# Performance work log

Measured on AMD Instinct MI355X. Metric: run time of the kernel, lower is better.

## Reference

```python
import jax, jax.numpy as jnp
import numpy as np

NUM_EXPERTS = 8
TOP_K = 2
D_IN = 1024
D_OUT = 1024
N_TOKENS = 8192


def setup_inputs() -> dict:
    key = jax.random.key(0)
    ks = jax.random.split(key, 7)
    s_in = 1.0 / np.sqrt(D_IN)
    s_out = 1.0 / np.sqrt(D_OUT)
    return {
        "x": jax.random.normal(ks[0], (N_TOKENS, D_IN), dtype=jnp.float32),
        # stacked expert params: fc1 [E, D_in, D_out], fc2 [E, D_out, D_out]
        "W1": jax.random.uniform(ks[1], (NUM_EXPERTS, D_IN, D_OUT), jnp.float32, -s_in, s_in),
        "b1": jax.random.uniform(ks[2], (NUM_EXPERTS, D_OUT), jnp.float32, -s_in, s_in),
        "W2": jax.random.uniform(ks[3], (NUM_EXPERTS, D_OUT, D_OUT), jnp.float32, -s_out, s_out),
        "b2": jax.random.uniform(ks[4], (NUM_EXPERTS, D_OUT), jnp.float32, -s_out, s_out),
        "Wg": jax.random.uniform(ks[5], (D_IN, NUM_EXPERTS), jnp.float32, -s_in, s_in),
        "bg": jax.random.uniform(ks[6], (NUM_EXPERTS,), jnp.float32, -s_in, s_in),
    }


def reference(x, W1, b1, W2, b2, Wg, bg):
    n = x.shape[0]
    # gating
    gate_logits = x @ Wg + bg                      # [N, E]
    gate_weights = jax.nn.softmax(gate_logits, axis=1)
    if TOP_K < NUM_EXPERTS:
        topk_vals, topk_idx = jax.lax.top_k(gate_weights, TOP_K)  # [N, K]
        rows = jnp.arange(n)[:, None]
        gate_weights = jnp.zeros_like(gate_weights).at[rows, topk_idx].set(topk_vals)
    # dense all-expert MLP fan-out (faithful to the original wasteful compute)
    h = jax.nn.relu(jnp.einsum('nd,edh->enh', x, W1) + b1[:, None, :])  # [E, N, H]
    y = jnp.einsum('enh,eho->eno', h, W2) + b2[:, None, :]               # [E, N, O]
    # weighted combine over experts
    out = jnp.einsum('ne,eno->no', gate_weights, y)                      # [N, O]
    return out
```

## Files before the change

kernel.cpp:

```cpp
#include <hip/hip_runtime.h>

#define NUM_E 8
#define N_TOK 8192
#define DIM 1024

typedef __attribute__((ext_vector_type(8))) short short8;
typedef __attribute__((ext_vector_type(4))) float f32x4;

__device__ __forceinline__ unsigned short f2bf(float f) {
  unsigned int u = __float_as_uint(f);
  u = (u + 0x7fffu + ((u >> 16) & 1u)) >> 16;
  return (unsigned short)u;
}

__device__ __forceinline__ void async16(const unsigned short* g, unsigned short* l) {
  __builtin_amdgcn_global_load_lds((const __attribute__((address_space(1))) void*)g,
                                   (__attribute__((address_space(3))) void*)l,
                                   16, 0, 0);
}

__global__ __launch_bounds__(256) void prep_kernel(
    const float* __restrict__ W1, const float* __restrict__ W2,
    unsigned short* __restrict__ W1T, unsigned short* __restrict__ W2T,
    const float* __restrict__ x, const float* __restrict__ Wg,
    const float* __restrict__ bg, int* __restrict__ tok_top,
    float2* __restrict__ tok_wts, unsigned short* __restrict__ xb) {
  __shared__ float s[64][65];
  if (blockIdx.x < 4096) {
    const int bx  = blockIdx.x;
    const int mat = bx >> 8;
    const int tk  = (bx >> 4) & 15;
    const int tn  = bx & 15;
    const float* src;
    unsigned short* dst;
    if (mat < 8) { src = W1 + (size_t)mat * (DIM * DIM); dst = W1T + (size_t)mat * (DIM * DIM); }
    else         { src = W2 + (size_t)(mat - 8) * (DIM * DIM); dst = W2T + (size_t)(mat - 8) * (DIM * DIM); }
    const int k0 = tk * 64, n0 = tn * 64;
    const int t = threadIdx.x;
    const int nr = t & 63, wr = t >> 6;
#pragma unroll
    for (int i = 0; i < 16; ++i) {
      int k = i * 4 + wr;
      s[nr][k] = src[(size_t)(k0 + k) * DIM + n0 + nr];
    }
    __syncthreads();
    const int kq = (t & 15) * 4, nw = t >> 4;
#pragma unroll
    for (int i = 0; i < 4; ++i) {
      int n = i * 16 + nw;
      ushort4 o;
      o.x = f2bf(s[n][kq + 0]); o.y = f2bf(s[n][kq + 1]);
      o.z = f2bf(s[n][kq + 2]); o.w = f2bf(s[n][kq + 3]);
      *(ushort4*)(dst + (size_t)(n0 + n) * DIM + k0 + kq) = o;
    }
  } else {
    const int wave = threadIdx.x >> 6;
    const int lane = threadIdx.x & 63;
    const int n = (blockIdx.x - 4096) * 4 + wave;
    const float4* xr = (const float4*)(x + (size_t)n * DIM);
    unsigned short* xbr = xb + (size_t)n * DIM;
    float acc[NUM_E];
#pragma unroll
    for (int e = 0; e < NUM_E; ++e) acc[e] = 0.f;
#pragma unroll
    for (int it = 0; it < 4; ++it) {
      float4 xv = xr[it * 64 + lane];
      const float4* wr = (const float4*)Wg + (size_t)(it * 256 + lane * 4) * 2;
      float xs[4] = {xv.x, xv.y, xv.z, xv.w};
      union { unsigned short u[4]; uint2 v; } oo;
      oo.u[0] = f2bf(xv.x); oo.u[1] = f2bf(xv.y);
      oo.u[2] = f2bf(xv.z); oo.u[3] = f2bf(xv.w);
      *(uint2*)(xbr + it * 256 + lane * 4) = oo.v;
#pragma unroll
      for (int dd = 0; dd < 4; ++dd) {
        float4 wa = wr[dd * 2 + 0];
        float4 wb = wr[dd * 2 + 1];
        acc[0] += xs[dd] * wa.x; acc[1] += xs[dd] * wa.y;
        acc[2] += xs[dd] * wa.z; acc[3] += xs[dd] * wa.w;
        acc[4] += xs[dd] * wb.x; acc[5] += xs[dd] * wb.y;
        acc[6] += xs[dd] * wb.z; acc[7] += xs[dd] * wb.w;
      }
    }
#pragma unroll
    for (int e = 0; e < NUM_E; ++e)
#pragma unroll
      for (int off = 32; off > 0; off >>= 1)
        acc[e] += __shfl_down(acc[e], off);
    if (lane == 0) {
      float p[NUM_E];
      float mx = -1e30f;
#pragma unroll
      for (int e = 0; e < NUM_E; ++e) { p[e] = acc[e] + bg[e]; mx = fmaxf(mx, p[e]); }
      float ss = 0.f;
#pragma unroll
      for (int e = 0; e < NUM_E; ++e) { p[e] = expf(p[e] - mx); ss += p[e]; }
      float inv = 1.f / ss;
      int i0 = 0;
#pragma unroll
      for (int e = 1; e < NUM_E; ++e) if (p[e] > p[i0]) i0 = e;
      int i1 = (i0 == 0) ? 1 : 0;
#pragma unroll
      for (int e = 0; e < NUM_E; ++e) if (e != i0 && p[e] > p[i1]) i1 = e;
      tok_top[n] = i0 | (i1 << 8);
      tok_wts[n] = make_float2(p[i0] * inv, p[i1] * inv);
    }
  }
}

__global__ __launch_bounds__(1024) void gate2_kernel(const int* __restrict__ tok_top,
                                                     const float2* __restrict__ tok_wts,
                                                     int* __restrict__ counts,
                                                     int* __restrict__ tok_idx,
                                                     float* __restrict__ tok_w) {
  const int e = blockIdx.x;
  const int t = threadIdx.x;
  const int lane = t & 63;
  const int wave = t >> 6;
  __shared__ int wsum[16];
  __shared__ int blocktot;
  int match[8];
  float w[8];
  int cnt = 0;
#pragma unroll
  for (int j = 0; j < 8; ++j) {
    int n = t * 8 + j;
    int top = tok_top[n];
    float2 ww = tok_wts[n];
    bool m0 = (top & 0xff) == e;
    bool m1 = ((top >> 8) & 0xff) == e;
    match[j] = (m0 || m1) ? 1 : 0;
    w[j] = m0 ? ww.x : ww.y;
    cnt += match[j];
  }
  int inc = cnt;
#pragma unroll
  for (int off = 1; off < 64; off <<= 1) {
    int v = __shfl_up(inc, off);
    if (lane >= off) inc += v;
  }
  if (lane == 63) wsum[wave] = inc;
  __syncthreads();
  if (t < 16) {
    int v = wsum[t];
    int s = v;
#pragma unroll
    for (int off = 1; off < 16; off <<= 1) {
      int u = __shfl_up(s, off);
      if (lane >= off) s += u;
    }
    wsum[t] = s - v;
    if (t == 15) blocktot = s;
  }
  __syncthreads();
  int slot = wsum[wave] + inc - cnt;
#pragma unroll
  for (int j = 0; j < 8; ++j) {
    if (match[j]) {
      tok_idx[e * N_TOK + slot] = t * 8 + j;
      tok_w[e * N_TOK + slot] = w[j];
      slot++;
    }
  }
  if (t == 0) counts[e] = blocktot;
}


template <bool FC1>
__global__ __launch_bounds__(256, 3) void moe_gemm_kernel(
    const unsigned short* __restrict__ A_src,
    const unsigned short* __restrict__ wT,
    const float* __restrict__ bias,
    const int* __restrict__ counts,
    const int* __restrict__ tok_idx,
    const float* __restrict__ tok_w,
    unsigned short* __restrict__ h_out,
    float* __restrict__ out)
{
  const int y = blockIdx.y;
  int e = -1, m0 = 0, base = 0;
  {
    int acc_tiles = 0, acc_rows = 0;
#pragma unroll
    for (int i = 0; i < NUM_E; ++i) {
      int c = counts[i];
      int t = (c + 127) >> 7;
      if (y >= acc_tiles && y < acc_tiles + t) {
        e = i; m0 = (y - acc_tiles) * 128; base = acc_rows;
      }
      acc_tiles += t;
      acc_rows += t * 128;
    }
  }
  if (e < 0) return;
  const int count = counts[e];
  const int n0 = blockIdx.x * 128;

  const int tid  = threadIdx.x;
  const int wave = tid >> 6;
  const int lane = tid & 63;
  const int l15  = lane & 15;
  const int quad = lane >> 4;
  const int wm   = wave & 1;
  const int wn   = wave >> 1;

  __shared__ unsigned short sA[2 * 4096];
  __shared__ unsigned short sB[2 * 4096];
  __shared__ int   s_tok[128];
  __shared__ float s_w[128];

  if (!FC1 && tid < 128) {
    int slot = m0 + tid;
    int cs = slot < count ? slot : count - 1;
    s_tok[tid] = tok_idx[e * N_TOK + cs];
    s_w[tid]   = slot < count ? tok_w[e * N_TOK + slot] : 0.f;
  }

  const int r0 = 32 * wave + l15;
  const int r1 = r0 + 16;
  size_t aOff0, aOff1;
  if (FC1) {
    int s0 = m0 + r0; s0 = s0 < count ? s0 : count - 1;
    int s1 = m0 + r1; s1 = s1 < count ? s1 : count - 1;
    aOff0 = (size_t)tok_idx[e * N_TOK + s0] * DIM;
    aOff1 = (size_t)tok_idx[e * N_TOK + s1] * DIM;
  } else {
    aOff0 = (size_t)(base + m0 + r0) * DIM;
    aOff1 = (size_t)(base + m0 + r1) * DIM;
  }
  const unsigned short* wte = wT + (size_t)e * DIM * DIM;
  const size_t bOff0 = (size_t)(n0 + r0) * DIM;
  const size_t bOff1 = (size_t)(n0 + r1) * DIM;
  const int kl = quad * 8;
  const int c0 = (2 * wave + 0) * 512;
  const int c1 = (2 * wave + 1) * 512;

  const f32x4 vzero = {0.f, 0.f, 0.f, 0.f};
  f32x4 acc[4][4];
#pragma unroll
  for (int i = 0; i < 4; ++i)
#pragma unroll
    for (int j = 0; j < 4; ++j) acc[i][j] = vzero;

  for (int k0 = 0; k0 < DIM; k0 += 64) {
    async16(A_src + aOff0 + k0 + kl,      &sA[c0]);
    async16(A_src + aOff1 + k0 + kl,      &sA[c1]);
    async16(A_src + aOff0 + k0 + 32 + kl, &sA[4096 + c0]);
    async16(A_src + aOff1 + k0 + 32 + kl, &sA[4096 + c1]);
    async16(wte + bOff0 + k0 + kl,        &sB[c0]);
    async16(wte + bOff1 + k0 + kl,        &sB[c1]);
    async16(wte + bOff0 + k0 + 32 + kl,   &sB[4096 + c0]);
    async16(wte + bOff1 + k0 + 32 + kl,   &sB[4096 + c1]);
    __syncthreads();
#pragma unroll
    for (int s = 0; s < 2; ++s) {
      short8 af[4], bfr[4];
#pragma unroll
      for (int i = 0; i < 4; ++i)
        af[i] = *(const short8*)&sA[s * 4096 + (wm * 4 + i) * 512 + lane * 8];
#pragma unroll
      for (int j = 0; j < 4; ++j)
        bfr[j] = *(const short8*)&sB[s * 4096 + (wn * 4 + j) * 512 + lane * 8];
#pragma unroll
      for (int i = 0; i < 4; ++i)
#pragma unroll
        for (int j = 0; j < 4; ++j)
          acc[i][j] = __builtin_amdgcn_mfma_f32_16x16x32_bf16(af[i], bfr[j], acc[i][j], 0, 0, 0);
    }
    __syncthreads();
  }

  float bv[4];
#pragma unroll
  for (int j = 0; j < 4; ++j)
    bv[j] = bias[e * DIM + n0 + (wn * 4 + j) * 16 + l15];

  if (FC1) {
#pragma unroll
    for (int i = 0; i < 4; ++i) {
      const int rbase = (wm * 4 + i) * 16 + quad * 4;
#pragma unroll
      for (int r = 0; r < 4; ++r) {
        const int slot = m0 + rbase + r;
        if (slot < count) {
          unsigned short* hp = h_out + (size_t)(base + slot) * DIM + n0;
#pragma unroll
          for (int j = 0; j < 4; ++j) {
            float v = acc[i][j][r] + bv[j];
            v = v > 0.f ? v : 0.f;
            hp[(wn * 4 + j) * 16 + l15] = f2bf(v);
          }
        }
      }
    }
  } else {
#pragma unroll
    for (int i = 0; i < 4; ++i) {
      const int rbase = (wm * 4 + i) * 16 + quad * 4;
#pragma unroll
      for (int r = 0; r < 4; ++r) {
        const int slot = m0 + rbase + r;
        if (slot < count) {
          const int rl = rbase + r;
          const int tok = s_tok[rl];
          const float w = s_w[rl];
          float* op = out + (size_t)tok * DIM + n0;
#pragma unroll
          for (int j = 0; j < 4; ++j) {
            float v = acc[i][j][r] + bv[j];
            atomicAdd(&op[(wn * 4 + j) * 16 + l15], w * v);
          }
        }
      }
    }
  }
}


extern "C" void kernel_launch(void* const* d_in, const int* in_sizes, int n_in,
                              void* d_out, int out_size, void* d_ws, size_t ws_size,
                              hipStream_t stream) {
  const float* x  = (const float*)d_in[0];
  const float* W1 = (const float*)d_in[1];
  const float* b1 = (const float*)d_in[2];
  const float* W2 = (const float*)d_in[3];
  const float* b2 = (const float*)d_in[4];
  const float* Wg = (const float*)d_in[5];
  const float* bg = (const float*)d_in[6];
  float* out = (float*)d_out;

  char* ws = (char*)d_ws;
  int*            counts  = (int*)(ws);
  int*            tok_idx = (int*)(ws + 1024);
  float*          tok_w   = (float*)(ws + 263168);
  unsigned short* xb      = (unsigned short*)(ws + 525312);
  unsigned short* w1t     = (unsigned short*)(ws + 525312 + 16777216ull);
  unsigned short* w2t     = (unsigned short*)(ws + 525312 + 2ull * 16777216ull);
  unsigned short* hb      = (unsigned short*)(ws + 525312 + 3ull * 16777216ull);
  size_t gate_off = 525312 + 3ull * 16777216ull + 35651584ull;
  int*            tok_top = (int*)(ws + gate_off);
  float2*         tok_wts = (float2*)(ws + gate_off + 32768);

  hipMemsetAsync(d_out, 0, (size_t)N_TOK * DIM * sizeof(float), stream);

  prep_kernel<<<4096 + 2048, 256, 0, stream>>>(W1, W2, w1t, w2t,
                                               x, Wg, bg, tok_top, tok_wts, xb);
  gate2_kernel<<<NUM_E, 1024, 0, stream>>>(tok_top, tok_wts, counts, tok_idx, tok_w);
  moe_gemm_kernel<true><<<dim3(8, 136), 256, 0, stream>>>(
      xb, w1t, b1, counts, tok_idx, tok_w, hb, nullptr);
  moe_gemm_kernel<false><<<dim3(8, 136), 256, 0, stream>>>(
      hb, w2t, b2, counts, tok_idx, tok_w, nullptr, out);
}
```

Baseline: 373.0 us.

## Vectorize weight transpose, remap GEMM blocks per XCD, raise occupancy

The weight transpose/convert kernel now reads float4 and writes 16-byte bf16 vectors instead of scalar loads and 8-byte stores, cutting memory instruction count. The grouped GEMM launch becomes a 1D grid whose block index is remapped so that each XCD gets a contiguous range of M tiles, with all 8 N tiles of an M tile on the same XCD, for better L2 reuse of A rows. Launch bounds are raised to 4 blocks per SM, which may force register pressure or spills. The transpose's LDS writes with the new pattern may introduce bank conflicts.

```diff
diff --git a/kernel.cpp b/kernel.cpp
--- a/kernel.cpp
+++ b/kernel.cpp
@@ -37,21 +37,29 @@
     else         { src = W2 + (size_t)(mat - 8) * (DIM * DIM); dst = W2T + (size_t)(mat - 8) * (DIM * DIM); }
     const int k0 = tk * 64, n0 = tn * 64;
     const int t = threadIdx.x;
-    const int nr = t & 63, wr = t >> 6;
-#pragma unroll
-    for (int i = 0; i < 16; ++i) {
-      int k = i * 4 + wr;
-      s[nr][k] = src[(size_t)(k0 + k) * DIM + n0 + nr];
+    {
+      const int rr = t >> 4;
+      const int c4 = (t & 15) * 4;
+#pragma unroll
+      for (int i = 0; i < 4; ++i) {
+        const int k = i * 16 + rr;
+        float4 v = *(const float4*)&src[(size_t)(k0 + k) * DIM + n0 + c4];
+        s[c4 + 0][k] = v.x; s[c4 + 1][k] = v.y;
+        s[c4 + 2][k] = v.z; s[c4 + 3][k] = v.w;
+      }
     }
     __syncthreads();
-    const int kq = (t & 15) * 4, nw = t >> 4;
-#pragma unroll
-    for (int i = 0; i < 4; ++i) {
-      int n = i * 16 + nw;
-      ushort4 o;
-      o.x = f2bf(s[n][kq + 0]); o.y = f2bf(s[n][kq + 1]);
-      o.z = f2bf(s[n][kq + 2]); o.w = f2bf(s[n][kq + 3]);
-      *(ushort4*)(dst + (size_t)(n0 + n) * DIM + k0 + kq) = o;
+    {
+      const int kq = (t & 7) * 8;
+      const int nn = t >> 3;
+#pragma unroll
+      for (int r = 0; r < 2; ++r) {
+        const int n = r * 32 + nn;
+        union { unsigned short us[8]; uint4 v; } o;
+#pragma unroll
+        for (int j = 0; j < 8; ++j) o.us[j] = f2bf(s[n][kq + j]);
+        *(uint4*)(dst + (size_t)(n0 + n) * DIM + k0 + kq) = o.v;
+      }
     }
   } else {
     const int wave = threadIdx.x >> 6;
@@ -166,7 +174,7 @@
 
 
 template <bool FC1>
-__global__ __launch_bounds__(256, 3) void moe_gemm_kernel(
+__global__ __launch_bounds__(256, 4) void moe_gemm_kernel(
     const unsigned short* __restrict__ A_src,
     const unsigned short* __restrict__ wT,
     const float* __restrict__ bias,
@@ -176,7 +184,11 @@
     unsigned short* __restrict__ h_out,
     float* __restrict__ out)
 {
-  const int y = blockIdx.y;
+  const int bid = blockIdx.x;
+  const int xcd = bid & 7;
+  const int mt  = xcd * 17 + (bid >> 6);
+  const int nt  = (bid >> 3) & 7;
+
   int e = -1, m0 = 0, base = 0;
   {
     int acc_tiles = 0, acc_rows = 0;
@@ -184,8 +196,8 @@
     for (int i = 0; i < NUM_E; ++i) {
       int c = counts[i];
       int t = (c + 127) >> 7;
-      if (y >= acc_tiles && y < acc_tiles + t) {
-        e = i; m0 = (y - acc_tiles) * 128; base = acc_rows;
+      if (mt >= acc_tiles && mt < acc_tiles + t) {
+        e = i; m0 = (mt - acc_tiles) * 128; base = acc_rows;
       }
       acc_tiles += t;
       acc_rows += t * 128;
@@ -193,7 +205,7 @@
   }
   if (e < 0) return;
   const int count = counts[e];
-  const int n0 = blockIdx.x * 128;
+  const int n0 = nt * 128;
 
   const int tid  = threadIdx.x;
   const int wave = tid >> 6;
@@ -345,8 +357,8 @@
   prep_kernel<<<4096 + 2048, 256, 0, stream>>>(W1, W2, w1t, w2t,
                                                x, Wg, bg, tok_top, tok_wts, xb);
   gate2_kernel<<<NUM_E, 1024, 0, stream>>>(tok_top, tok_wts, counts, tok_idx, tok_w);
-  moe_gemm_kernel<true><<<dim3(8, 136), 256, 0, stream>>>(
+  moe_gemm_kernel<true><<<1088, 256, 0, stream>>>(
       xb, w1t, b1, counts, tok_idx, tok_w, hb, nullptr);
-  moe_gemm_kernel<false><<<dim3(8, 136), 256, 0, stream>>>(
+  moe_gemm_kernel<false><<<1088, 256, 0, stream>>>(
       hb, w2t, b2, counts, tok_idx, tok_w, nullptr, out);
 }
```

After: 368.4 us. Within noise of the previous version (-1.2%).
